# Performance work log

Hardware: AMD Instinct MI355X
Metric: run time of the kernel (lower is better)

The kernel has to match this reference:

```python
import jax, jax.numpy as jnp
import numpy as np

B, D, F, N = 16, 8, 2, 512
E = D + F


def setup_inputs() -> dict:
    key = jax.random.key(0)
    ks = jax.random.split(key, 8)
    obs_mean = jax.random.normal(ks[0], (B, D), jnp.float32)
    action_mean = jax.random.normal(ks[1], (B, F), jnp.float32)
    # joint PSD input covariance over x_tilde = [x, u], then slice blocks
    A = 0.1 * jax.random.normal(ks[2], (B, E, E), jnp.float32)
    J = A @ jnp.swapaxes(A, -1, -2) / E + 0.01 * jnp.eye(E, dtype=jnp.float32)
    obs_var = J[:, :D, :D]
    action_var = J[:, D:, D:]
    cross_cov = J[:, :D, D:]
    X_train = jax.random.normal(ks[3], (N, E), jnp.float32)
    ell = jax.random.uniform(ks[4], (D, E), jnp.float32, 0.7, 1.5)
    alpha_sq = jax.random.uniform(ks[5], (D,), jnp.float32, 0.5, 1.5)
    sigma_sq_eps = 0.01 * jnp.ones((D,), jnp.float32)
    y = 0.1 * jax.random.normal(ks[6], (D, N), jnp.float32)

    def per_dim(ell_a, a2, s2, y_a):
        Xs = X_train / ell_a
        sq = jnp.sum((Xs[:, None, :] - Xs[None, :, :]) ** 2, axis=-1)
        Kn = a2 * jnp.exp(-0.5 * sq) + (s2 + 1e-6) * jnp.eye(N, dtype=jnp.float32)
        invK = jnp.linalg.inv(Kn)
        return invK, invK @ y_a

    inv_K, beta = jax.vmap(per_dim)(ell, alpha_sq, sigma_sq_eps, y)
    return {
        "obs_mean": obs_mean, "obs_var": obs_var,
        "action_mean": action_mean, "action_var": action_var,
        "cross_cov": cross_cov,
        "X_train": X_train, "ell": ell, "alpha_sq": alpha_sq,
        "sigma_sq_eps": sigma_sq_eps, "beta": beta, "inv_K": inv_K,
    }


def reference(obs_mean, obs_var, action_mean, action_var, cross_cov,
              X_train, ell, alpha_sq, sigma_sq_eps, beta, inv_K):
    """PILCO moment matching (Deisenroth & Rasmussen 2011, Eqs. 10-23).

    One SE-ARD GP per output dim a predicts the residual Delta_a; a Gaussian
    joint belief N(mu, Sigma) over x_tilde = [x, u] is propagated analytically.
    Returns (mu_next [B,D], Sigma_next [B,D,D]).
    """
    f32 = jnp.float32
    mu = jnp.concatenate([obs_mean, action_mean], axis=-1)              # [B,E]
    top = jnp.concatenate([obs_var, cross_cov], axis=-1)                # [B,D,E]
    bot = jnp.concatenate([jnp.swapaxes(cross_cov, -1, -2), action_var], axis=-1)
    Sigma = jnp.concatenate([top, bot], axis=-2)                        # [B,E,E]

    nu = X_train[None, :, :] - mu[:, None, :]                           # [B,N,E]
    ell2 = ell ** 2                                                     # [D,E]
    iLam = 1.0 / ell2                                                   # [D,E]
    Lam = jax.vmap(jnp.diag)(ell2)                                      # [D,E,E]

    # ---- predictive mean (Eqs. 10-12): q_ai = a2 |Sigma iLam + I|^{-1/2}
    #      exp(-0.5 nu_i^T (Sigma+Lam)^{-1} nu_i)
    Amat = Sigma[:, None, :, :] + Lam[None, :, :, :]                    # [B,D,E,E]
    Ainv = jnp.linalg.inv(Amat)
    logdetA = jnp.linalg.slogdet(Amat)[1]                               # [B,D]
    logdetLam = jnp.sum(jnp.log(ell2), axis=-1)                         # [D]
    quad = jnp.einsum('bne,bdef,bnf->bdn', nu, Ainv, nu)
    q = alpha_sq[None, :, None] * jnp.exp(
        0.5 * (logdetLam[None, :] - logdetA)[..., None] - 0.5 * quad)   # [B,D,N]
    mu_delta = jnp.einsum('dn,bdn->bd', beta, q)                        # [B,D]

    # ---- input-output covariance Cov[x_tilde, Delta_a]
    w = jnp.einsum('dn,bdn,bne->bde', beta, q, nu)                      # [B,D,E]
    V = jnp.einsum('bef,bdfg,bdg->bde', Sigma, Ainv, w)                 # [B,D,E]

    # ---- predictive covariance (Eqs. 20-23)
    logk = jnp.log(alpha_sq)[None, :, None] - 0.5 * jnp.einsum(
        'bne,de->bdn', nu ** 2, iLam)                                   # [B,D,N]
    P = nu[:, None, :, :] * iLam[None, :, None, :]                      # [B,D,N,E]
    eyeE = jnp.eye(E, dtype=f32)

    rows, traces = [], []
    for a in range(D):  # loop over obs dims (structurally distinct pairs)
        iLsum = iLam[a][None, :] + iLam                                 # [D,E]
        R = Sigma[:, None, :, :] * iLsum[None, :, None, :] + eyeE       # [B,D,E,E]
        S = jnp.linalg.solve(R, jnp.broadcast_to(Sigma[:, None], R.shape))
        logdetR = jnp.linalg.slogdet(R)[1]                              # [B,D]
        Pa = P[:, a]                                                    # [B,N,E]
        d_a = jnp.einsum('bie,bdef,bif->bdi', Pa, S, Pa)                # [B,D,N]
        d_b = jnp.einsum('bdje,bdef,bdjf->bdj', P, S, P)                # [B,D,N]
        m = jnp.einsum('bie,bdef,bdjf->bdij', Pa, S, P)                 # [B,D,N,N]
        c_a = logk[:, a][:, None, :] + 0.5 * d_a
        c_b = logk + 0.5 * d_b
        Q = jnp.exp(c_a[..., :, None] + m + c_b[..., None, :]
                    - 0.5 * logdetR[..., None, None])                   # [B,D,N,N]
        rows.append(jnp.einsum('i,bdij,dj->bd', beta[a], Q, beta))
        traces.append(jnp.einsum('ij,bij->b', inv_K[a], Q[:, a]))

    EDD = jnp.stack(rows, axis=1)                                       # [B,D,D]
    tr = jnp.stack(traces, axis=1)                                      # [B,D]
    Sigma_delta = EDD - mu_delta[:, :, None] * mu_delta[:, None, :]
    Sigma_delta = 0.5 * (Sigma_delta + jnp.swapaxes(Sigma_delta, -1, -2))
    diag_corr = alpha_sq[None, :] - tr + sigma_sq_eps[None, :]          # [B,D]
    Sigma_delta = Sigma_delta + jax.vmap(jnp.diag)(diag_corr)

    # ---- next-state moments: x_next = x + Delta
    C_xd = jnp.swapaxes(V[..., :D], 1, 2)                               # [B,Dx,Dd]
    mu_next = obs_mean + mu_delta
    Sigma_next = obs_var + Sigma_delta + C_xd + jnp.swapaxes(C_xd, -1, -2)
    return mu_next, Sigma_next
```

## Files before the change

### kernel.cpp

```cpp
#include <hip/hip_runtime.h>
#include <math.h>

#define B 16
#define D 8
#define FDIM 2
#define N 512
#define E 10
#define NP36 36
#define GJW (2*E)
#define NT 4
#define TIL 128
#define NQ (NP36*B*NT)
#define NSYS (NP36*B + B*D)
#define NPREPB NSYS
#define LOG2E 1.44269504088896340736f
#define KA 12
#define TRI(e, f) ((e) * E - (e) * ((e) - 1) / 2 + ((f) - (e)))

#define OFF_MUD  0
#define OFF_V    128
#define OFF_EDDP 1408
#define OFF_TRP  3712
#define OFF_W    4224
#define OFF_CA   61824
#define OFF_CB   356736

typedef _Float16 f16x4 __attribute__((ext_vector_type(4)));
typedef float f32x4 __attribute__((ext_vector_type(4)));

__device__ __forceinline__ float exp2_hw(float x) {
  float r;
  __asm__ __volatile__("v_exp_f32 %0, %1" : "=v"(r) : "v"(x));
  return r;
}

__device__ __forceinline__ void decode_pair(int p36, int* pa, int* pd) {
  int a = 0, rem = p36;
  while (rem >= D - a) { rem -= (D - a); a++; }
  *pa = a; *pd = a + rem;
}

__device__ __forceinline__ float wave_reduce(float v) {
#pragma unroll
  for (int off = 32; off > 0; off >>= 1) v += __shfl_down(v, off);
  return v;
}

__device__ __forceinline__ void wsync() {
  __asm__ __volatile__("" ::: "memory");
  __builtin_amdgcn_wave_barrier();
  __asm__ __volatile__("" ::: "memory");
}

__device__ __forceinline__ float gj_wave(float (*M)[GJW], int lane) {
  float pivs[E];
#pragma unroll
  for (int k = 0; k < E; k++) {
    wsync();
    int pr = k;
    float best = fabsf(M[k][k]);
#pragma unroll
    for (int r = 1; r < E; r++) {
      if (r > k) {
        float v = fabsf(M[r][k]);
        if (v > best) { best = v; pr = r; }
      }
    }
    pivs[k] = M[pr][k];
    wsync();
    float tk = 0.f, pw = 0.f;
    if (lane < GJW) {
      float piv = M[pr][k];
      pw = M[pr][lane] / piv;
      tk = M[k][lane];
    }
    wsync();
    if (lane < GJW) {
      M[pr][lane] = tk;
      M[k][lane]  = pw;
    }
    wsync();
    float cf[4], pv[4], cur[4];
    int rr[4], cc[4];
#pragma unroll
    for (int t = 0; t < 4; t++) {
      int idx = lane + t * 64;
      if (idx < E * GJW) {
        int r = idx / GJW, c = idx - r * GJW;
        rr[t] = r; cc[t] = c;
        cf[t]  = M[r][k];
        pv[t]  = M[k][c];
        cur[t] = M[r][c];
      } else {
        rr[t] = k; cc[t] = 0; cf[t] = 0.f; pv[t] = 0.f; cur[t] = 0.f;
      }
    }
    wsync();
#pragma unroll
    for (int t = 0; t < 4; t++) {
      int idx = lane + t * 64;
      if (idx < E * GJW && rr[t] != k) {
        M[rr[t]][cc[t]] = fmaf(-cf[t], pv[t], cur[t]);
      }
    }
  }
  wsync();
  float ld = 0.f;
#pragma unroll
  for (int k = 0; k < E; k++) ld += logf(fabsf(pivs[k]));
  return ld;
}

__global__ __launch_bounds__(256) void k_prep(
    const float* __restrict__ obs_mean, const float* __restrict__ obs_var,
    const float* __restrict__ action_mean, const float* __restrict__ action_var,
    const float* __restrict__ cross_cov, const float* __restrict__ X,
    const float* __restrict__ ell, const float* __restrict__ alpha_sq,
    const float* __restrict__ beta, float* __restrict__ ws) {
  __shared__ float M[4][E][GJW];
  __shared__ float sSig[4][E * E];
  __shared__ float sMu[4][E], siLa[4][E], siLd[4][E];

  int tid = threadIdx.x;
  int wid = tid >> 6, lane = tid & 63;
  int sid = blockIdx.x;

  if (sid >= NP36 * B) {
    if (wid != 0) return;
    int bd = sid - NP36 * B;
    int b = bd >> 3, d = bd & 7;
    if (lane < E) {
      sMu[0][lane] = (lane < D) ? obs_mean[b * D + lane]
                                : action_mean[b * FDIM + lane - D];
    }
    for (int idx = lane; idx < E * E; idx += 64) {
      int e = idx / E, f = idx % E;
      float v;
      if (e < D && f < D)      v = obs_var[(b * D + e) * D + f];
      else if (e < D)          v = cross_cov[(b * D + e) * FDIM + (f - D)];
      else if (f < D)          v = cross_cov[(b * D + f) * FDIM + (e - D)];
      else                     v = action_var[(b * FDIM + (e - D)) * FDIM + (f - D)];
      sSig[0][idx] = v;
    }
    wsync();
    for (int idx = lane; idx < E * GJW; idx += 64) {
      int r = idx / GJW, c = idx % GJW;
      float v;
      if (c < E) {
        v = sSig[0][r * E + c];
        if (r == c) { float l = ell[d * E + r]; v += l * l; }
      } else {
        v = (c - E == r) ? 1.0f : 0.0f;
      }
      M[0][r][c] = v;
    }
    float lda = gj_wave(M[0], lane);
    float At2[55];
#pragma unroll
    for (int e = 0; e < E; e++) {
#pragma unroll
      for (int f = e; f < E; f++) {
        float s = M[0][e][E + f];
        At2[TRI(e, f)] = (e == f) ? s : (s + s);
      }
    }
    float a2 = alpha_sq[d];
    float logdetLam = 0.0f;
#pragma unroll
    for (int e = 0; e < E; e++) { float l = ell[d * E + e]; logdetLam += logf(l * l); }
    float c0 = 0.5f * (logdetLam - lda);
    float acc_mu = 0.0f, acc_w[E];
#pragma unroll
    for (int e = 0; e < E; e++) acc_w[e] = 0.0f;
#pragma unroll
    for (int t = 0; t < 8; t++) {
      int n = lane + t * 64;
      float x[E];
#pragma unroll
      for (int e = 0; e < E; e++) x[e] = X[n * E + e] - sMu[0][e];
      float quad = 0.0f;
#pragma unroll
      for (int e = 0; e < E; e++) {
        float te = 0.0f;
#pragma unroll
        for (int f = e; f < E; f++) te = fmaf(At2[TRI(e, f)], x[f], te);
        quad = fmaf(x[e], te, quad);
      }
      float qval = a2 * __expf(c0 - 0.5f * quad);
      float bq = beta[d * N + n] * qval;
      acc_mu += bq;
#pragma unroll
      for (int e = 0; e < E; e++) acc_w[e] += bq * x[e];
    }
    acc_mu = wave_reduce(acc_mu);
#pragma unroll
    for (int e = 0; e < E; e++) acc_w[e] = wave_reduce(acc_w[e]);
    if (lane == 0) {
      ws[OFF_MUD + b * D + d] = acc_mu;
      float u[E];
#pragma unroll
      for (int f = 0; f < E; f++) {
        float s = 0.0f;
#pragma unroll
        for (int g = 0; g < E; g++) s += M[0][f][E + g] * acc_w[g];
        u[f] = s;
      }
#pragma unroll
      for (int e = 0; e < E; e++) {
        float s = 0.0f;
#pragma unroll
        for (int f = 0; f < E; f++) s += sSig[0][e * E + f] * u[f];
        ws[OFF_V + (b * D + d) * E + e] = s;
      }
    }
    return;
  }

  int p36 = sid >> 4, b = sid & 15;
  int a, d;
  decode_pair(p36, &a, &d);
  int pb = p36 * B + b;
  if (lane < E) {
    sMu[wid][lane] = (lane < D) ? obs_mean[b * D + lane]
                                : action_mean[b * FDIM + lane - D];
    float la = ell[a * E + lane]; siLa[wid][lane] = 1.0f / (la * la);
    float ld = ell[d * E + lane]; siLd[wid][lane] = 1.0f / (ld * ld);
  }
  for (int idx = lane; idx < E * E; idx += 64) {
    int e = idx / E, f = idx % E;
    float v;
    if (e < D && f < D)      v = obs_var[(b * D + e) * D + f];
    else if (e < D)          v = cross_cov[(b * D + e) * FDIM + (f - D)];
    else if (f < D)          v = cross_cov[(b * D + f) * FDIM + (e - D)];
    else                     v = action_var[(b * FDIM + (e - D)) * FDIM + (f - D)];
    sSig[wid][idx] = v;
  }
  wsync();
  for (int idx = lane; idx < E * GJW; idx += 64) {
    int r = idx / GJW, c = idx % GJW;
    float v;
    if (c < E) v = sSig[wid][r * E + c] * (siLa[wid][c] + siLd[wid][c]) + ((r == c) ? 1.0f : 0.0f);
    else       v = sSig[wid][r * E + (c - E)];
    M[wid][r][c] = v;
  }
  float ldr = gj_wave(M[wid], lane);
  float St2[55];
#pragma unroll
  for (int e = 0; e < E; e++) {
#pragma unroll
    for (int f = e; f < E; f++) {
      float s = M[wid][e][E + f];
      St2[TRI(e, f)] = (e == f) ? s : (s + s);
    }
  }
  float lga = logf(alpha_sq[a]);
  float lgd = logf(alpha_sq[d]);
  if (wid == 0) {
    for (int idx = lane; idx < E * E; idx += 64) {
      int e = idx / E, f = idx % E;
      ws[OFF_W + pb * (E * E) + idx] = LOG2E * M[0][e][E + f] * siLa[0][e] * siLd[0][f];
    }
  }
#pragma unroll
  for (int t = 0; t < 2; t++) {
    int n = lane + wid * 64 + t * 256;
    float pa_[E], pd_[E];
    float s2a = 0.0f, s2b = 0.0f;
#pragma unroll
    for (int e = 0; e < E; e++) {
      float xe = X[n * E + e] - sMu[wid][e];
      pa_[e] = xe * siLa[wid][e];
      pd_[e] = xe * siLd[wid][e];
      s2a += xe * pa_[e];
      s2b += xe * pd_[e];
    }
    float da = 0.0f, db = 0.0f;
#pragma unroll
    for (int e = 0; e < E; e++) {
      float ta = 0.0f, td = 0.0f;
#pragma unroll
      for (int f = e; f < E; f++) {
        float s = St2[TRI(e, f)];
        ta = fmaf(s, pa_[f], ta);
        td = fmaf(s, pd_[f], td);
      }
      da = fmaf(pa_[e], ta, da);
      db = fmaf(pd_[e], td, db);
    }
    ws[OFF_CA + pb * N + n] = LOG2E * (lga - 0.5f * s2a + 0.5f * da - 0.5f * ldr);
    ws[OFF_CB + pb * N + n] = LOG2E * (lgd - 0.5f * s2b + 0.5f * db);
  }
}

__global__ __launch_bounds__(256) void k_q(
    const float* __restrict__ obs_mean, const float* __restrict__ action_mean,
    const float* __restrict__ X, const float* __restrict__ beta,
    const float* __restrict__ invK, float* __restrict__ ws) {
  __shared__ __attribute__((aligned(16))) _Float16 snh[N * KA];
  __shared__ __attribute__((aligned(16))) _Float16 snl[N * KA];
  __shared__ __attribute__((aligned(16))) _Float16 sTh[TIL * KA + 8];
  __shared__ __attribute__((aligned(16))) _Float16 sTl[TIL * KA + 8];
  __shared__ float sW[E * E];
  __shared__ float sMu[E];
  __shared__ __attribute__((aligned(16))) float sba[TIL];
  __shared__ float redw[8];

  int tid = threadIdx.x;
  int bx = blockIdx.x;
  int tile = bx & (NT - 1);
  int rest = bx >> 2;
  int b = rest & (B - 1);
  int p36 = rest >> 4;
  int a, d;
  decode_pair(p36, &a, &d);
  int pb = p36 * B + b;
  bool diag = (a == d);
  int i0 = tile * TIL;

  if (tid < E) sMu[tid] = (tid < D) ? obs_mean[b * D + tid] : action_mean[b * FDIM + tid - D];
  if (tid < E * E) sW[tid] = ws[OFF_W + pb * (E * E) + tid];
  if (tid < TIL) sba[tid] = beta[a * N + i0 + tid];
  if (tid < 8) { sTh[TIL * KA + tid] = (_Float16)0.f; sTl[TIL * KA + tid] = (_Float16)0.f; }
  __syncthreads();

  for (int jj = tid; jj < N; jj += 256) {
    float v[KA];
#pragma unroll
    for (int e = 0; e < E; e++) v[e] = X[jj * E + e] - sMu[e];
    v[10] = 1.0f;
    v[11] = ws[OFF_CB + (size_t)pb * N + jj];
#pragma unroll
    for (int k = 0; k < KA; k++) {
      _Float16 h = (_Float16)v[k];
      snh[jj * KA + k] = h;
      snl[jj * KA + k] = (_Float16)(v[k] - (float)h);
    }
  }

  {
    int il = tid >> 1;
    int k0 = (tid & 1) * 6;
    float nu[E];
#pragma unroll
    for (int e = 0; e < E; e++) nu[e] = X[(i0 + il) * E + e] - sMu[e];
#pragma unroll
    for (int kk = 0; kk < 6; kk++) {
      int k = k0 + kk;
      float v;
      if (k < E) {
        v = 0.f;
#pragma unroll
        for (int e = 0; e < E; e++) v = fmaf(nu[e], sW[e * E + k], v);
      } else if (k == E) {
        v = ws[OFF_CA + (size_t)pb * N + i0 + il];
      } else {
        v = 1.0f;
      }
      _Float16 h = (_Float16)v;
      sTh[il * KA + k] = h;
      sTl[il * KA + k] = (_Float16)(v - (float)h);
    }
  }
  __syncthreads();

  int lane = tid & 63;
  int w = tid >> 6;
  int c = lane & 15;
  int kg = lane >> 4;
  bool kval = (kg < 3);
  int koff = kg * 4;
  float accR = 0.f;
  float accT0 = 0.f, accT1 = 0.f, accT2 = 0.f, accT3 = 0.f;
  const float* invKa = invK + (size_t)a * N * N;
  const f32x4 zero4 = {0.f, 0.f, 0.f, 0.f};

  f16x4 Ah[8], Al[8];
  f32x4 bav[8];
#pragma unroll
  for (int it = 0; it < 8; it++) {
    Ah[it] = *(const f16x4*)&sTh[(it * 16 + c) * KA + koff];
    Al[it] = *(const f16x4*)&sTl[(it * 16 + c) * KA + koff];
    bav[it] = *(const f32x4*)&sba[it * 16 + koff];
  }

  for (int jt8 = 0; jt8 < 8; jt8++) {
    int jt = (w << 3) + jt8;
    int j = (jt << 4) + c;
    f16x4 Bh = {(_Float16)0.f, (_Float16)0.f, (_Float16)0.f, (_Float16)0.f};
    f16x4 Bl = {(_Float16)0.f, (_Float16)0.f, (_Float16)0.f, (_Float16)0.f};
    if (kval) {
      Bh = *(const f16x4*)&snh[j * KA + koff];
      Bl = *(const f16x4*)&snl[j * KA + koff];
    }
    float bd = beta[d * N + j];
    const float* kvrow = invKa + (size_t)j * N + i0 + koff;
#pragma unroll
    for (int it = 0; it < 8; it++) {
      f32x4 m = __builtin_amdgcn_mfma_f32_16x16x16f16(Ah[it], Bh, zero4, 0, 0, 0);
      m = __builtin_amdgcn_mfma_f32_16x16x16f16(Ah[it], Bl, m, 0, 0, 0);
      m = __builtin_amdgcn_mfma_f32_16x16x16f16(Al[it], Bh, m, 0, 0, 0);
      float q0 = exp2_hw(m[0]);
      float q1 = exp2_hw(m[1]);
      float q2 = exp2_hw(m[2]);
      float q3 = exp2_hw(m[3]);
      float t = bav[it][0] * q0;
      t = fmaf(bav[it][1], q1, t);
      t = fmaf(bav[it][2], q2, t);
      t = fmaf(bav[it][3], q3, t);
      accR = fmaf(bd, t, accR);
      if (diag) {
        f32x4 r = *(const f32x4*)(kvrow + it * 16);
        accT0 = fmaf(r[0], q0, accT0);
        accT1 = fmaf(r[1], q1, accT1);
        accT2 = fmaf(r[2], q2, accT2);
        accT3 = fmaf(r[3], q3, accT3);
      }
    }
  }

  {
    float rr = wave_reduce(accR);
    int wid = tid >> 6, ln = tid & 63;
    if (ln == 0) redw[wid] = rr;
    if (diag) {
      float rt = wave_reduce((accT0 + accT1) + (accT2 + accT3));
      if (ln == 0) redw[4 + wid] = rt;
    }
    __syncthreads();
    if (tid == 0) {
      ws[OFF_EDDP + (p36 * B + b) * NT + tile] = redw[0] + redw[1] + redw[2] + redw[3];
      if (diag)
        ws[OFF_TRP + (a * B + b) * NT + tile] = redw[4] + redw[5] + redw[6] + redw[7];
    }
  }
}

__global__ __launch_bounds__(64) void k_final(
    const float* __restrict__ obs_mean, const float* __restrict__ obs_var,
    const float* __restrict__ alpha_sq, const float* __restrict__ sigma_sq_eps,
    const float* __restrict__ ws, float* __restrict__ out) {
  int b = blockIdx.x;
  int tid = threadIdx.x;
  const float* mud = ws + OFF_MUD + b * D;
  if (tid < D) out[b * D + tid] = obs_mean[b * D + tid] + mud[tid];
  if (tid < D * D) {
    int i = tid / D, j = tid % D;
    int a = i < j ? i : j;
    int dd = i < j ? j : i;
    int p36 = a * D - a * (a - 1) / 2 + (dd - a);
    float edd = 0.0f;
#pragma unroll
    for (int tt = 0; tt < NT; tt++) edd += ws[OFF_EDDP + (p36 * B + b) * NT + tt];
    float sd = edd - mud[i] * mud[j];
    if (i == j) {
      float tr = 0.0f;
#pragma unroll
      for (int tt = 0; tt < NT; tt++) tr += ws[OFF_TRP + (i * B + b) * NT + tt];
      sd += alpha_sq[i] - tr + sigma_sq_eps[i];
    }
    const float* V = ws + OFF_V;
    float cxd = V[(b * D + j) * E + i];
    float cdx = V[(b * D + i) * E + j];
    out[B * D + b * D * D + tid] = obs_var[b * D * D + tid] + sd + cxd + cdx;
  }
}

extern "C" void kernel_launch(void* const* d_in, const int* in_sizes, int n_in,
                              void* d_out, int out_size, void* d_ws, size_t ws_size,
                              hipStream_t stream) {
  const float* obs_mean     = (const float*)d_in[0];
  const float* obs_var      = (const float*)d_in[1];
  const float* action_mean  = (const float*)d_in[2];
  const float* action_var   = (const float*)d_in[3];
  const float* cross_cov    = (const float*)d_in[4];
  const float* X_train      = (const float*)d_in[5];
  const float* ell          = (const float*)d_in[6];
  const float* alpha_sq     = (const float*)d_in[7];
  const float* sigma_sq_eps = (const float*)d_in[8];
  const float* beta         = (const float*)d_in[9];
  const float* inv_K        = (const float*)d_in[10];
  float* out = (float*)d_out;
  float* ws = (float*)d_ws;

  k_prep<<<NPREPB, 256, 0, stream>>>(obs_mean, obs_var, action_mean, action_var,
                                     cross_cov, X_train, ell, alpha_sq, beta, ws);
  k_q<<<NQ, 256, 0, stream>>>(obs_mean, action_mean, X_train, beta, inv_K, ws);
  k_final<<<B, 64, 0, stream>>>(obs_mean, obs_var, alpha_sq, sigma_sq_eps, ws, out);
}
```

Before: 142.1 us.

## Split Q kernel over j halves and build A operands in registers

Each (pair, batch, i-tile) block is now split into two blocks over the j dimension, which doubles the grid and halves the per-block j loop and its shared staging. The A-side operand (nu·W, c_a, 1) is now computed directly into registers per lane instead of being staged through shared memory. This adds redundant X loads and W FMAs across lanes, and doubles the number of partial sums the final kernel must reduce. Workspace offsets are shifted to make room for the larger partial arrays.

```diff
diff --git a/kernel.cpp b/kernel.cpp
--- a/kernel.cpp
+++ b/kernel.cpp
@@ -10,7 +10,9 @@
 #define GJW (2*E)
 #define NT 4
 #define TIL 128
-#define NQ (NP36*B*NT)
+#define JH 2
+#define JTIL 256
+#define NQ (NP36*B*NT*JH)
 #define NSYS (NP36*B + B*D)
 #define NPREPB NSYS
 #define LOG2E 1.44269504088896340736f
@@ -20,10 +22,10 @@
 #define OFF_MUD  0
 #define OFF_V    128
 #define OFF_EDDP 1408
-#define OFF_TRP  3712
-#define OFF_W    4224
-#define OFF_CA   61824
-#define OFF_CB   356736
+#define OFF_TRP  6016
+#define OFF_W    7040
+#define OFF_CA   64640
+#define OFF_CB   359552
 
 typedef _Float16 f16x4 __attribute__((ext_vector_type(4)));
 typedef float f32x4 __attribute__((ext_vector_type(4)));
@@ -296,10 +298,8 @@
     const float* __restrict__ obs_mean, const float* __restrict__ action_mean,
     const float* __restrict__ X, const float* __restrict__ beta,
     const float* __restrict__ invK, float* __restrict__ ws) {
-  __shared__ __attribute__((aligned(16))) _Float16 snh[N * KA];
-  __shared__ __attribute__((aligned(16))) _Float16 snl[N * KA];
-  __shared__ __attribute__((aligned(16))) _Float16 sTh[TIL * KA + 8];
-  __shared__ __attribute__((aligned(16))) _Float16 sTl[TIL * KA + 8];
+  __shared__ __attribute__((aligned(16))) _Float16 snh[JTIL * KA];
+  __shared__ __attribute__((aligned(16))) _Float16 snl[JTIL * KA];
   __shared__ float sW[E * E];
   __shared__ float sMu[E];
   __shared__ __attribute__((aligned(16))) float sba[TIL];
@@ -307,8 +307,9 @@
 
   int tid = threadIdx.x;
   int bx = blockIdx.x;
-  int tile = bx & (NT - 1);
-  int rest = bx >> 2;
+  int jh = bx & (JH - 1);
+  int tile = (bx >> 1) & (NT - 1);
+  int rest = bx >> 3;
   int b = rest & (B - 1);
   int p36 = rest >> 4;
   int a, d;
@@ -316,52 +317,28 @@
   int pb = p36 * B + b;
   bool diag = (a == d);
   int i0 = tile * TIL;
+  int j0 = jh * JTIL;
 
   if (tid < E) sMu[tid] = (tid < D) ? obs_mean[b * D + tid] : action_mean[b * FDIM + tid - D];
   if (tid < E * E) sW[tid] = ws[OFF_W + pb * (E * E) + tid];
   if (tid < TIL) sba[tid] = beta[a * N + i0 + tid];
-  if (tid < 8) { sTh[TIL * KA + tid] = (_Float16)0.f; sTl[TIL * KA + tid] = (_Float16)0.f; }
   __syncthreads();
 
-  for (int jj = tid; jj < N; jj += 256) {
+  {
+    int jl = tid;
+    int jg = j0 + jl;
     float v[KA];
 #pragma unroll
-    for (int e = 0; e < E; e++) v[e] = X[jj * E + e] - sMu[e];
+    for (int e = 0; e < E; e++) v[e] = X[jg * E + e] - sMu[e];
     v[10] = 1.0f;
-    v[11] = ws[OFF_CB + (size_t)pb * N + jj];
+    v[11] = ws[OFF_CB + (size_t)pb * N + jg];
 #pragma unroll
     for (int k = 0; k < KA; k++) {
       _Float16 h = (_Float16)v[k];
-      snh[jj * KA + k] = h;
-      snl[jj * KA + k] = (_Float16)(v[k] - (float)h);
-    }
-  }
-
-  {
-    int il = tid >> 1;
-    int k0 = (tid & 1) * 6;
-    float nu[E];
-#pragma unroll
-    for (int e = 0; e < E; e++) nu[e] = X[(i0 + il) * E + e] - sMu[e];
-#pragma unroll
-    for (int kk = 0; kk < 6; kk++) {
-      int k = k0 + kk;
-      float v;
-      if (k < E) {
-        v = 0.f;
-#pragma unroll
-        for (int e = 0; e < E; e++) v = fmaf(nu[e], sW[e * E + k], v);
-      } else if (k == E) {
-        v = ws[OFF_CA + (size_t)pb * N + i0 + il];
-      } else {
-        v = 1.0f;
-      }
-      _Float16 h = (_Float16)v;
-      sTh[il * KA + k] = h;
-      sTl[il * KA + k] = (_Float16)(v - (float)h);
-    }
-  }
-  __syncthreads();
+      snh[jl * KA + k] = h;
+      snl[jl * KA + k] = (_Float16)(v[k] - (float)h);
+    }
+  }
 
   int lane = tid & 63;
   int w = tid >> 6;
@@ -369,31 +346,61 @@
   int kg = lane >> 4;
   bool kval = (kg < 3);
   int koff = kg * 4;
+  f16x4 Ah[8], Al[8];
+  f32x4 bav[8];
+#pragma unroll
+  for (int it = 0; it < 8; it++) {
+    if (kval) {
+      int row = i0 + it * 16 + c;
+      float nu[E];
+#pragma unroll
+      for (int e = 0; e < E; e++) nu[e] = X[row * E + e] - sMu[e];
+      float t4[4];
+#pragma unroll
+      for (int kk = 0; kk < 4; kk++) {
+        int k = koff + kk;
+        float v;
+        if (k < E) {
+          v = 0.f;
+#pragma unroll
+          for (int e = 0; e < E; e++) v = fmaf(nu[e], sW[e * E + k], v);
+        } else if (k == E) {
+          v = ws[OFF_CA + (size_t)pb * N + row];
+        } else {
+          v = 1.0f;
+        }
+        t4[kk] = v;
+      }
+#pragma unroll
+      for (int kk = 0; kk < 4; kk++) {
+        _Float16 h = (_Float16)t4[kk];
+        Ah[it][kk] = h;
+        Al[it][kk] = (_Float16)(t4[kk] - (float)h);
+      }
+    } else {
+      Ah[it] = (f16x4){(_Float16)0.f, (_Float16)0.f, (_Float16)0.f, (_Float16)0.f};
+      Al[it] = (f16x4){(_Float16)0.f, (_Float16)0.f, (_Float16)0.f, (_Float16)0.f};
+    }
+    bav[it] = *(const f32x4*)&sba[it * 16 + koff];
+  }
+  __syncthreads();
+
   float accR = 0.f;
   float accT0 = 0.f, accT1 = 0.f, accT2 = 0.f, accT3 = 0.f;
   const float* invKa = invK + (size_t)a * N * N;
   const f32x4 zero4 = {0.f, 0.f, 0.f, 0.f};
 
-  f16x4 Ah[8], Al[8];
-  f32x4 bav[8];
-#pragma unroll
-  for (int it = 0; it < 8; it++) {
-    Ah[it] = *(const f16x4*)&sTh[(it * 16 + c) * KA + koff];
-    Al[it] = *(const f16x4*)&sTl[(it * 16 + c) * KA + koff];
-    bav[it] = *(const f32x4*)&sba[it * 16 + koff];
-  }
-
-  for (int jt8 = 0; jt8 < 8; jt8++) {
-    int jt = (w << 3) + jt8;
-    int j = (jt << 4) + c;
+  for (int jt4 = 0; jt4 < 4; jt4++) {
+    int jl = ((w << 2) + jt4) * 16 + c;
+    int jg = j0 + jl;
     f16x4 Bh = {(_Float16)0.f, (_Float16)0.f, (_Float16)0.f, (_Float16)0.f};
     f16x4 Bl = {(_Float16)0.f, (_Float16)0.f, (_Float16)0.f, (_Float16)0.f};
     if (kval) {
-      Bh = *(const f16x4*)&snh[j * KA + koff];
-      Bl = *(const f16x4*)&snl[j * KA + koff];
-    }
-    float bd = beta[d * N + j];
-    const float* kvrow = invKa + (size_t)j * N + i0 + koff;
+      Bh = *(const f16x4*)&snh[jl * KA + koff];
+      Bl = *(const f16x4*)&snl[jl * KA + koff];
+    }
+    float bd = beta[d * N + jg];
+    const float* kvrow = invKa + (size_t)jg * N + i0 + koff;
 #pragma unroll
     for (int it = 0; it < 8; it++) {
       f32x4 m = __builtin_amdgcn_mfma_f32_16x16x16f16(Ah[it], Bh, zero4, 0, 0, 0);
@@ -428,9 +435,11 @@
     }
     __syncthreads();
     if (tid == 0) {
-      ws[OFF_EDDP + (p36 * B + b) * NT + tile] = redw[0] + redw[1] + redw[2] + redw[3];
+      ws[OFF_EDDP + (p36 * B + b) * (NT * JH) + tile * JH + jh] =
+          redw[0] + redw[1] + redw[2] + redw[3];
       if (diag)
-        ws[OFF_TRP + (a * B + b) * NT + tile] = redw[4] + redw[5] + redw[6] + redw[7];
+        ws[OFF_TRP + (a * B + b) * (NT * JH) + tile * JH + jh] =
+            redw[4] + redw[5] + redw[6] + redw[7];
     }
   }
 }
@@ -450,12 +459,14 @@
     int p36 = a * D - a * (a - 1) / 2 + (dd - a);
     float edd = 0.0f;
 #pragma unroll
-    for (int tt = 0; tt < NT; tt++) edd += ws[OFF_EDDP + (p36 * B + b) * NT + tt];
+    for (int tt = 0; tt < NT * JH; tt++)
+      edd += ws[OFF_EDDP + (p36 * B + b) * (NT * JH) + tt];
     float sd = edd - mud[i] * mud[j];
     if (i == j) {
       float tr = 0.0f;
 #pragma unroll
-      for (int tt = 0; tt < NT; tt++) tr += ws[OFF_TRP + (i * B + b) * NT + tt];
+      for (int tt = 0; tt < NT * JH; tt++)
+        tr += ws[OFF_TRP + (i * B + b) * (NT * JH) + tt];
       sd += alpha_sq[i] - tr + sigma_sq_eps[i];
     }
     const float* V = ws + OFF_V;
```

Measured after the change: 197.6 us. +39.1%, slower.
